# Performance work log

Hardware: AMD Instinct MI355X
Metric: run time of the kernel (lower is better)

## Reference

```python
import jax, jax.numpy as jnp
import numpy as np

DIM = 256; HEADS = 8; DK = 64; DV = 64; FH = 32; FW = 32; B = 16
INK = HEADS * DK; INV = HEADS * DV; N = FH * FW
SCALE = DK ** -0.5; EPS = 1e-5


def _pos_indices():
    pos = np.stack(np.meshgrid(np.arange(FH), np.arange(FW), indexing='ij'), axis=-1).reshape(-1, 2)
    rel = np.abs(pos[:, None, :] - pos[None, :, :])  # [N,N,2]
    return jnp.asarray(rel[..., 0] * FW + rel[..., 1], jnp.int32)  # [N,N]


def _bn(x, g, b, m, v):
    # eval-mode BatchNorm2d over channel axis 1
    s = (g / jnp.sqrt(v + EPS))
    return x * s[None, :, None, None] + (b - m * s)[None, :, None, None]


def setup_inputs() -> dict:
    key = jax.random.key(0)
    ks = jax.random.split(key, 24)
    f32 = jnp.float32
    def bn_params(k, c):
        k1, k2, k3, k4 = jax.random.split(k, 4)
        return (jax.random.normal(k1, (c,), f32) * 0.1 + 1.0,
                jax.random.normal(k2, (c,), f32) * 0.1,
                jax.random.normal(k3, (c,), f32) * 0.1,
                jax.random.uniform(k4, (c,), f32) + 0.5)
    gq, bq, mq, vq = bn_params(ks[1], INK)
    gk, bk, mk, vk = bn_params(ks[3], INK)
    gv, bv, mv, vv = bn_params(ks[5], INV)
    go, bo, mo, vo = bn_params(ks[7], DIM)
    return {
        'x': jax.random.normal(ks[0], (B, DIM, FH, FW), f32),
        'wq': jax.random.normal(ks[2], (INK, DIM), f32) * (DIM ** -0.5),
        'gq': gq, 'bq': bq, 'mq': mq, 'vq': vq,
        'wk': jax.random.normal(ks[4], (INK, DIM), f32) * (DIM ** -0.5),
        'gk': gk, 'bk': bk, 'mk': mk, 'vk': vk,
        'wv': jax.random.normal(ks[6], (INV, DIM), f32) * (DIM ** -0.5),
        'gv': gv, 'bv': bv, 'mv': mv, 'vv': vv,
        'emb': jax.random.normal(ks[8], (N, HEADS), f32) * 0.02,
        'w_out': jax.random.normal(ks[9], (DIM, INV), f32) * (INV ** -0.5),
        'b_out': jax.random.normal(ks[10], (DIM,), f32) * 0.02,
        'go': go, 'bo': bo, 'mo': mo, 'vo': vo,
        'pos_indices': _pos_indices(),
    }


def reference(x, wq, gq, bq, mq, vq, wk, gk, bk, mk, vk, wv, gv, bv, mv, vv,
              emb, w_out, b_out, go, bo, mo, vo, pos_indices):
    b = x.shape[0]
    # 1x1 conv == channel matmul
    q = _bn(jnp.einsum('bchw,oc->bohw', x, wq), gq, bq, mq, vq)
    k = _bn(jnp.einsum('bchw,oc->bohw', x, wk), gk, bk, mk, vk)
    v = _bn(jnp.einsum('bchw,oc->bohw', x, wv), gv, bv, mv, vv)
    # 'b (h d) x y -> b h (x y) d'
    def split_heads(t, d):
        return t.reshape(b, HEADS, d, N).transpose(0, 1, 3, 2)
    q = split_heads(q, DK); k = split_heads(k, DK); v = split_heads(v, DV)
    dots = jnp.einsum('bhid,bhjd->bhij', q, k) * SCALE  # [b,h,N,N]
    bias = emb[pos_indices]                               # [N,N,h] gather
    dots = dots + jnp.transpose(bias, (2, 0, 1))[None] / SCALE
    attn = jax.nn.softmax(dots, axis=-1)
    out = jnp.einsum('bhij,bhjd->bhid', attn, v)
    out = out.transpose(0, 1, 3, 2).reshape(b, INV, FH, FW)  # 'b h (x y) d -> b (h d) x y'
    hs = out * jnp.clip(out + 3.0, 0.0, 6.0) / 6.0           # Hardswish
    y = jnp.einsum('bchw,oc->bohw', hs, w_out) + b_out[None, :, None, None]
    return _bn(y, go, bo, mo, vo)
```

## Files before the change

### kernel.cpp

```cpp
#include <hip/hip_runtime.h>

typedef __attribute__((ext_vector_type(4))) float f32x4;
typedef __attribute__((ext_vector_type(8))) _Float16 f16x8;
typedef __attribute__((ext_vector_type(4))) _Float16 f16x4;

static __device__ __forceinline__ f32x4 mfma16f(f16x8 a, f16x8 b, f32x4 c) {
    return __builtin_amdgcn_mfma_f32_16x16x32_f16(a, b, c, 0, 0, 0);
}

__global__ __launch_bounds__(256) void prep(
    const float* __restrict__ x,
    const float* __restrict__ s0, const float* __restrict__ s1,
    const float* __restrict__ s2, const float* __restrict__ s3,
    _Float16* __restrict__ d0h, _Float16* __restrict__ d0l,
    _Float16* __restrict__ d1h, _Float16* __restrict__ d1l,
    _Float16* __restrict__ d2h, _Float16* __restrict__ d2l,
    _Float16* __restrict__ d3h, _Float16* __restrict__ d3l,
    _Float16* __restrict__ xth, _Float16* __restrict__ xtl)
{
    __shared__ float lt[32][36];
    const int t = threadIdx.x;
    const int bid = blockIdx.x;
    if (bid < 2048) {
        const int seg = bid >> 9;
        const int i = (bid & 511) * 256 + t;
        const float* src = (seg == 0) ? s0 : (seg == 1) ? s1 : (seg == 2) ? s2 : s3;
        _Float16* dh = (seg == 0) ? d0h : (seg == 1) ? d1h : (seg == 2) ? d2h : d3h;
        _Float16* dl = (seg == 0) ? d0l : (seg == 1) ? d1l : (seg == 2) ? d2l : d3l;
        const float f = src[i];
        const _Float16 h = (_Float16)f;
        dh[i] = h;
        dl[i] = (_Float16)(f - (float)h);
    } else {
        const int bid2 = bid - 2048;
        const int c0 = (bid2 & 7) * 32, hw0 = ((bid2 >> 3) & 31) * 32, b = bid2 >> 8;
        {
            const int cl = t >> 3, hw4 = (t & 7) * 4;
            *(f32x4*)&lt[cl][hw4] = *(const f32x4*)&x[((size_t)(b * 256 + c0 + cl)) * 1024 + hw0 + hw4];
        }
        __syncthreads();
        {
            const int hwl = t >> 3, c4 = (t & 7) * 4;
            f16x4 hv, lv;
#pragma unroll
            for (int e = 0; e < 4; ++e) {
                const float f = lt[c4 + e][hwl];
                const _Float16 h = (_Float16)f;
                hv[e] = h;
                lv[e] = (_Float16)(f - (float)h);
            }
            const size_t off = ((size_t)(b * 1024 + hw0 + hwl)) * 256 + c0 + c4;
            *(f16x4*)(xth + off) = hv;
            *(f16x4*)(xtl + off) = lv;
        }
    }
}

__global__ __launch_bounds__(256) void qkv_mfma(
    const _Float16* __restrict__ xth, const _Float16* __restrict__ xtl,
    const _Float16* __restrict__ wqh, const _Float16* __restrict__ wql,
    const _Float16* __restrict__ wkh, const _Float16* __restrict__ wkl,
    const _Float16* __restrict__ wvh, const _Float16* __restrict__ wvl,
    const float* __restrict__ gq, const float* __restrict__ bq, const float* __restrict__ mq, const float* __restrict__ vq,
    const float* __restrict__ gk, const float* __restrict__ bk, const float* __restrict__ mk, const float* __restrict__ vk,
    const float* __restrict__ gv, const float* __restrict__ bv, const float* __restrict__ mv, const float* __restrict__ vv,
    _Float16* __restrict__ qh, _Float16* __restrict__ ql,
    _Float16* __restrict__ kh,
    _Float16* __restrict__ vt)
{
    __shared__ _Float16 Ah[128][72];
    __shared__ _Float16 Al[128][72];
    __shared__ float sc_l[128], tc_l[128];

    const int t = threadIdx.x;
    const int bn = blockIdx.x;
    const int m0 = blockIdx.y * 128;
    const int proj = bn >> 2;
    const int o0 = (bn & 3) * 128;
    const int bimg = m0 >> 10;
    const int nb = m0 & 1023;

    const _Float16* Wh = (proj == 0) ? wqh : (proj == 1) ? wkh : wvh;
    const _Float16* Wl = (proj == 0) ? wql : (proj == 1) ? wkl : wvl;
    const float* G  = (proj == 0) ? gq : (proj == 1) ? gk : gv;
    const float* Bt = (proj == 0) ? bq : (proj == 1) ? bk : bv;
    const float* Mn = (proj == 0) ? mq : (proj == 1) ? mk : mv;
    const float* Vr = (proj == 0) ? vq : (proj == 1) ? vk : vv;

    if (t < 128) {
        const int o = o0 + t;
        float s = G[o] / sqrtf(Vr[o] + 1e-5f);
        float tt = Bt[o] - Mn[o] * s;
        if (proj == 0) { s *= 0.125f; tt *= 0.125f; }
        sc_l[t] = s; tc_l[t] = tt;
    }

    const int wave = t >> 6, lane = t & 63;
    const int quad = lane >> 4, l16 = lane & 15;
    const int wm = (wave >> 1) * 64, wn = (wave & 1) * 64;

    f32x4 acc[4][4] = {};

    for (int c0 = 0; c0 < 256; c0 += 64) {
        __syncthreads();
        {
            int r = t >> 3;
            const int cs = (t & 7) * 8;
#pragma unroll
            for (int p = 0; p < 4; ++p, r += 32) {
                const size_t off = ((size_t)(bimg * 1024 + nb + r)) * 256 + c0 + cs;
                *(f16x8*)&Ah[r][cs] = *(const f16x8*)(xth + off);
                *(f16x8*)&Al[r][cs] = *(const f16x8*)(xtl + off);
            }
        }
        __syncthreads();
#pragma unroll
        for (int kk = 0; kk < 2; ++kk) {
            f16x8 ah[4], al[4], bh[4], bl[4];
#pragma unroll
            for (int mi = 0; mi < 4; ++mi) {
                ah[mi] = *(const f16x8*)&Ah[wm + mi * 16 + l16][kk * 32 + quad * 8];
                al[mi] = *(const f16x8*)&Al[wm + mi * 16 + l16][kk * 32 + quad * 8];
            }
#pragma unroll
            for (int nj = 0; nj < 4; ++nj) {
                const size_t off = ((size_t)(o0 + wn + nj * 16 + l16)) * 256 + c0 + kk * 32 + quad * 8;
                bh[nj] = *(const f16x8*)(Wh + off);
                if (proj < 2) bl[nj] = *(const f16x8*)(Wl + off);
            }
            if (proj < 2) {
#pragma unroll
                for (int nj = 0; nj < 4; ++nj)
#pragma unroll
                    for (int mi = 0; mi < 4; ++mi) {
                        acc[nj][mi] = mfma16f(bh[nj], ah[mi], acc[nj][mi]);
                        acc[nj][mi] = mfma16f(bh[nj], al[mi], acc[nj][mi]);
                        acc[nj][mi] = mfma16f(bl[nj], ah[mi], acc[nj][mi]);
                    }
            } else {
#pragma unroll
                for (int mi = 0; mi < 4; ++mi)
#pragma unroll
                    for (int nj = 0; nj < 4; ++nj) {
                        acc[mi][nj] = mfma16f(ah[mi], bh[nj], acc[mi][nj]);
                        acc[mi][nj] = mfma16f(al[mi], bh[nj], acc[mi][nj]);
                    }
            }
        }
    }

    if (proj < 2) {
        _Float16* Oh = (proj == 0) ? qh : kh;
#pragma unroll
        for (int nj = 0; nj < 4; ++nj) {
            const int olb = wn + nj * 16 + quad * 4;
            const int ob = o0 + olb;
            const int head = ob >> 6, d0 = ob & 63;
#pragma unroll
            for (int mi = 0; mi < 4; ++mi) {
                const int n = nb + wm + mi * 16 + l16;
                f16x4 hv, lv;
#pragma unroll
                for (int rr = 0; rr < 4; ++rr) {
                    const float val = acc[nj][mi][rr] * sc_l[olb + rr] + tc_l[olb + rr];
                    const _Float16 h = (_Float16)val;
                    hv[rr] = h;
                    lv[rr] = (_Float16)(val - (float)h);
                }
                const size_t off = (((size_t)(bimg * 8 + head)) * 1024 + n) * 64 + d0;
                *(f16x4*)(Oh + off) = hv;
                if (proj == 0) *(f16x4*)(ql + off) = lv;
            }
        }
    } else {
#pragma unroll
        for (int nj = 0; nj < 4; ++nj) {
            const int olb = wn + nj * 16 + l16;
            const int o = o0 + olb;
            const int head = o >> 6, d = o & 63;
            const float s = sc_l[olb], tt = tc_l[olb];
#pragma unroll
            for (int mi = 0; mi < 4; ++mi) {
                const int n0 = nb + wm + mi * 16 + quad * 4;
                f16x4 v4;
#pragma unroll
                for (int rr = 0; rr < 4; ++rr) v4[rr] = (_Float16)(acc[mi][nj][rr] * s + tt);
                *(f16x4*)(vt + (((size_t)(bimg * 8 + head)) * 64 + d) * 1024 + n0) = v4;
            }
        }
    }
}

__global__ __launch_bounds__(256, 3) void attn_mfma(
    const _Float16* __restrict__ qh, const _Float16* __restrict__ ql,
    const _Float16* __restrict__ kh,
    const _Float16* __restrict__ vt,
    const float* __restrict__ emb,
    _Float16* __restrict__ hsh)
{
    __shared__ float    emb_s[1024];
    __shared__ _Float16 kth[64][76];
    __shared__ _Float16 vts[64][76];
    __shared__ _Float16 pt[128][76];

    const int t = threadIdx.x;
    const int bid = blockIdx.x;
    const int bh = bid & 127, qb = bid >> 7;
    const int b = bh >> 3, h = bh & 7;
    const int wave = t >> 6, lane = t & 63;
    const int quad = lane >> 4, l16 = lane & 15;
    const int q0 = qb * 128 + wave * 32;
    const float L2E = 1.44269504f;

    for (int i = t; i < 1024; i += 256) emb_s[i] = (8.0f * emb[i * 8 + h] - 12.0f) * L2E;

    const size_t base = (size_t)bh * 65536;

    f16x8 qfh[2][2], qfl[2][2];
#pragma unroll
    for (int mi = 0; mi < 2; ++mi)
#pragma unroll
        for (int kk = 0; kk < 2; ++kk) {
            const size_t off = base + (size_t)(q0 + mi * 16 + l16) * 64 + kk * 32 + quad * 8;
            qfh[mi][kk] = *(const f16x8*)(qh + off);
            qfl[mi][kk] = *(const f16x8*)(ql + off);
        }

    int xiv[2][4], dy0[2][4], dy1[2][4];
#pragma unroll
    for (int mi = 0; mi < 2; ++mi)
#pragma unroll
        for (int r = 0; r < 4; ++r) {
            const int ig = q0 + mi * 16 + quad * 4 + r;
            const int xi = ig >> 5, yi = ig & 31;
            xiv[mi][r] = xi;
            dy0[mi][r] = abs(yi - l16);
            dy1[mi][r] = abs(yi - 16 - l16);
        }

    const int sr = t >> 3;
    const int scs = (t & 7) * 8;
    const int rv = t >> 2;
    const int cv = (t & 3) * 16;

    f16x8 pkh[2], pvv[2];
#pragma unroll
    for (int p = 0; p < 2; ++p) {
        pkh[p] = *(const f16x8*)(kh + base + (size_t)(p * 32 + sr) * 64 + scs);
        pvv[p] = *(const f16x8*)(vt + base + (size_t)rv * 1024 + cv + p * 8);
    }

    f32x4 ao[2][4] = {};
    float lsum[2][4] = {};

    for (int jb = 0; jb < 16; ++jb) {
        __syncthreads();
#pragma unroll
        for (int p = 0; p < 2; ++p) {
            *(f16x8*)&kth[p * 32 + sr][scs] = pkh[p];
            *(f16x8*)&vts[rv][cv + p * 8] = pvv[p];
        }
        __syncthreads();
        if (jb < 15) {
#pragma unroll
            for (int p = 0; p < 2; ++p) {
                pkh[p] = *(const f16x8*)(kh + base + (size_t)((jb + 1) * 64 + p * 32 + sr) * 64 + scs);
                pvv[p] = *(const f16x8*)(vt + base + (size_t)rv * 1024 + (jb + 1) * 64 + cv + p * 8);
            }
        }

        f32x4 as[2][4] = {};
#pragma unroll
        for (int kk = 0; kk < 2; ++kk) {
            f16x8 kfh[4];
#pragma unroll
            for (int nj = 0; nj < 4; ++nj)
                kfh[nj] = *(const f16x8*)&kth[nj * 16 + l16][kk * 32 + quad * 8];
#pragma unroll
            for (int mi = 0; mi < 2; ++mi)
#pragma unroll
                for (int nj = 0; nj < 4; ++nj) {
                    as[mi][nj] = mfma16f(qfh[mi][kk], kfh[nj], as[mi][nj]);
                    as[mi][nj] = mfma16f(qfl[mi][kk], kfh[nj], as[mi][nj]);
                }
        }

        const int xj0 = jb * 2, xj1 = jb * 2 + 1;
#pragma unroll
        for (int mi = 0; mi < 2; ++mi) {
#pragma unroll
            for (int r = 0; r < 4; ++r) {
                const int dxa = abs(xiv[mi][r] - xj0) << 5;
                const int dxb = abs(xiv[mi][r] - xj1) << 5;
                const int prow = wave * 32 + mi * 16 + quad * 4 + r;
                const float p0 = exp2f(fmaf(as[mi][0][r], L2E, emb_s[dxa + dy0[mi][r]]));
                const float p1 = exp2f(fmaf(as[mi][1][r], L2E, emb_s[dxa + dy1[mi][r]]));
                const float p2 = exp2f(fmaf(as[mi][2][r], L2E, emb_s[dxb + dy0[mi][r]]));
                const float p3 = exp2f(fmaf(as[mi][3][r], L2E, emb_s[dxb + dy1[mi][r]]));
                lsum[mi][r] += (p0 + p1) + (p2 + p3);
                pt[prow][0 * 16 + l16] = (_Float16)p0;
                pt[prow][1 * 16 + l16] = (_Float16)p1;
                pt[prow][2 * 16 + l16] = (_Float16)p2;
                pt[prow][3 * 16 + l16] = (_Float16)p3;
            }
        }

#pragma unroll
        for (int kk = 0; kk < 2; ++kk) {
            f16x8 pa[2], vf[4];
#pragma unroll
            for (int mi = 0; mi < 2; ++mi)
                pa[mi] = *(const f16x8*)&pt[wave * 32 + mi * 16 + l16][kk * 32 + quad * 8];
#pragma unroll
            for (int dj = 0; dj < 4; ++dj)
                vf[dj] = *(const f16x8*)&vts[dj * 16 + l16][kk * 32 + quad * 8];
#pragma unroll
            for (int mi = 0; mi < 2; ++mi)
#pragma unroll
                for (int dj = 0; dj < 4; ++dj)
                    ao[mi][dj] = mfma16f(pa[mi], vf[dj], ao[mi][dj]);
        }
    }

#pragma unroll
    for (int mi = 0; mi < 2; ++mi) {
#pragma unroll
        for (int r = 0; r < 4; ++r) {
            float l = lsum[mi][r];
#pragma unroll
            for (int msk = 1; msk < 16; msk <<= 1)
                l += __shfl_xor(l, msk, 64);
            const float inv = 1.0f / l;
            const int ig = q0 + mi * 16 + quad * 4 + r;
#pragma unroll
            for (int dj = 0; dj < 4; ++dj) {
                const float o = ao[mi][dj][r] * inv;
                const float hsw = o * fminf(fmaxf(o + 3.0f, 0.0f), 6.0f) * (1.0f / 6.0f);
                hsh[((size_t)(b * 1024 + ig)) * 512 + h * 64 + dj * 16 + l16] = (_Float16)hsw;
            }
        }
    }
}

__global__ __launch_bounds__(256) void out_mfma(
    const _Float16* __restrict__ hsh,
    const _Float16* __restrict__ woh, const _Float16* __restrict__ wol,
    const float* __restrict__ b_out, const float* __restrict__ go, const float* __restrict__ bo,
    const float* __restrict__ mo, const float* __restrict__ vo, float* __restrict__ y)
{
    __shared__ _Float16 Ah[64][136];

    const int t = threadIdx.x;
    const int m0 = blockIdx.x * 64;
    const int o0 = blockIdx.y * 128;
    const int bimg = m0 >> 10, nb = m0 & 1023;
    const int wave = t >> 6, lane = t & 63;
    const int quad = lane >> 4, l16 = lane & 15;
    const int wm = (wave >> 1) * 32, wn = (wave & 1) * 64;

    f32x4 acc[2][4] = {};
    f16x8 bh[4], bl[4], nbh[4], nbl[4];

#pragma unroll
    for (int nj = 0; nj < 4; ++nj) {
        const size_t off = ((size_t)(o0 + wn + nj * 16 + l16)) * 512 + quad * 8;
        bh[nj] = *(const f16x8*)(woh + off);
        bl[nj] = *(const f16x8*)(wol + off);
    }

#pragma unroll
    for (int it = 0; it < 16; ++it) {
        const int c0 = (it >> 2) * 128, kk = it & 3;
        if (kk == 0) {
            __syncthreads();
            const int cs = (t & 7) * 16;
#pragma unroll
            for (int p = 0; p < 2; ++p) {
                const int r = (t >> 3) + p * 32;
                *(f16x8*)&Ah[r][cs]     = *(const f16x8*)(hsh + ((size_t)(m0 + r)) * 512 + c0 + cs);
                *(f16x8*)&Ah[r][cs + 8] = *(const f16x8*)(hsh + ((size_t)(m0 + r)) * 512 + c0 + cs + 8);
            }
            __syncthreads();
        }
        if (it < 15) {
            const int nit = it + 1;
            const int nc0 = (nit >> 2) * 128, nkk = nit & 3;
#pragma unroll
            for (int nj = 0; nj < 4; ++nj) {
                const size_t off = ((size_t)(o0 + wn + nj * 16 + l16)) * 512 + nc0 + nkk * 32 + quad * 8;
                nbh[nj] = *(const f16x8*)(woh + off);
                nbl[nj] = *(const f16x8*)(wol + off);
            }
        }
        f16x8 ah[2];
#pragma unroll
        for (int mi = 0; mi < 2; ++mi)
            ah[mi] = *(const f16x8*)&Ah[wm + mi * 16 + l16][kk * 32 + quad * 8];
#pragma unroll
        for (int mi = 0; mi < 2; ++mi)
#pragma unroll
            for (int nj = 0; nj < 4; ++nj) {
                acc[mi][nj] = mfma16f(ah[mi], bh[nj], acc[mi][nj]);
                acc[mi][nj] = mfma16f(ah[mi], bl[nj], acc[mi][nj]);
            }
#pragma unroll
        for (int nj = 0; nj < 4; ++nj) { bh[nj] = nbh[nj]; bl[nj] = nbl[nj]; }
    }

#pragma unroll
    for (int nj = 0; nj < 4; ++nj) {
        const int o = o0 + wn + nj * 16 + l16;
        const float s = go[o] / sqrtf(vo[o] + 1e-5f);
        const float tt = bo[o] - mo[o] * s;
        const float bf = b_out[o];
#pragma unroll
        for (int mi = 0; mi < 2; ++mi) {
            const int hw = nb + wm + mi * 16 + quad * 4;
            f32x4 v4;
#pragma unroll
            for (int rr = 0; rr < 4; ++rr) v4[rr] = (acc[mi][nj][rr] + bf) * s + tt;
            *(f32x4*)&y[((size_t)(bimg * 256 + o)) * 1024 + hw] = v4;
        }
    }
}

extern "C" void kernel_launch(void* const* d_in, const int* in_sizes, int n_in,
                              void* d_out, int out_size, void* d_ws, size_t ws_size,
                              hipStream_t stream) {
    const float* x     = (const float*)d_in[0];
    const float* wq    = (const float*)d_in[1];
    const float* gq    = (const float*)d_in[2];
    const float* bq    = (const float*)d_in[3];
    const float* mq    = (const float*)d_in[4];
    const float* vq    = (const float*)d_in[5];
    const float* wk    = (const float*)d_in[6];
    const float* gk    = (const float*)d_in[7];
    const float* bk    = (const float*)d_in[8];
    const float* mk    = (const float*)d_in[9];
    const float* vk    = (const float*)d_in[10];
    const float* wv    = (const float*)d_in[11];
    const float* gv    = (const float*)d_in[12];
    const float* bv    = (const float*)d_in[13];
    const float* mv    = (const float*)d_in[14];
    const float* vv    = (const float*)d_in[15];
    const float* emb   = (const float*)d_in[16];
    const float* w_out = (const float*)d_in[17];
    const float* b_out = (const float*)d_in[18];
    const float* go    = (const float*)d_in[19];
    const float* bo    = (const float*)d_in[20];
    const float* mo    = (const float*)d_in[21];
    const float* vo    = (const float*)d_in[22];

    _Float16* us = (_Float16*)d_ws;
    _Float16* xth = us;
    _Float16* xtl = us + 4194304;
    _Float16* hsh = us;
    _Float16* wsp = us + 16777216;
    _Float16* wqh = wsp,            *wql = wsp + 131072;
    _Float16* wkh = wsp + 262144,   *wkl = wsp + 393216;
    _Float16* wvh = wsp + 524288,   *wvl = wsp + 655360;
    _Float16* woh = wsp + 786432,   *wol = wsp + 917504;
    _Float16* qv  = us + 17825792;
    _Float16* qhw = qv,             *qlw = qv + 8388608;
    _Float16* khw = qv + 16777216;
    _Float16* vtw = qv + 33554432;

    prep<<<6144, 256, 0, stream>>>(x, wq, wk, wv, w_out,
                                   wqh, wql, wkh, wkl, wvh, wvl, woh, wol,
                                   xth, xtl);

    qkv_mfma<<<dim3(12, 128), 256, 0, stream>>>(
        xth, xtl, wqh, wql, wkh, wkl, wvh, wvl,
        gq, bq, mq, vq, gk, bk, mk, vk, gv, bv, mv, vv,
        qhw, qlw, khw, vtw);

    attn_mfma<<<1024, 256, 0, stream>>>(
        qhw, qlw, khw, vtw, emb, hsh);

    out_mfma<<<dim3(256, 2), 256, 0, stream>>>(
        hsh, woh, wol, b_out, go, bo, mo, vo, (float*)d_out);
}
```

Before: 304.6 us.

## Compute transposed scores so softmax probs feed PV MFMA from registers

The QK^T MFMA now takes K as the A operand and Q as the B operand. The resulting transposed score fragment lines up directly with the A-operand layout of a 16x16x16 f16 MFMA for the P·V product. This removes the shared-memory P tile (pt) and its store/load round-trip, and cuts LDS use, which may raise occupancy. In exchange it uses the smaller-K 16x16x16 MFMA, gathers emb_s with per-element index math, and reworks the row-sum reduction with extra shuffles.

```diff
diff --git a/kernel.cpp b/kernel.cpp
--- a/kernel.cpp
+++ b/kernel.cpp
@@ -201,7 +201,6 @@
     __shared__ float    emb_s[1024];
     __shared__ _Float16 kth[64][76];
     __shared__ _Float16 vts[64][76];
-    __shared__ _Float16 pt[128][76];
 
     const int t = threadIdx.x;
     const int bid = blockIdx.x;
@@ -226,17 +225,13 @@
             qfl[mi][kk] = *(const f16x8*)(ql + off);
         }
 
-    int xiv[2][4], dy0[2][4], dy1[2][4];
-#pragma unroll
-    for (int mi = 0; mi < 2; ++mi)
-#pragma unroll
-        for (int r = 0; r < 4; ++r) {
-            const int ig = q0 + mi * 16 + quad * 4 + r;
-            const int xi = ig >> 5, yi = ig & 31;
-            xiv[mi][r] = xi;
-            dy0[mi][r] = abs(yi - l16);
-            dy1[mi][r] = abs(yi - 16 - l16);
-        }
+    int xi[2], yi[2];
+#pragma unroll
+    for (int mi = 0; mi < 2; ++mi) {
+        const int ig = q0 + mi * 16 + l16;
+        xi[mi] = ig >> 5;
+        yi[mi] = ig & 31;
+    }
 
     const int sr = t >> 3;
     const int scs = (t & 7) * 8;
@@ -251,7 +246,7 @@
     }
 
     f32x4 ao[2][4] = {};
-    float lsum[2][4] = {};
+    float lsum[2] = {};
 
     for (int jb = 0; jb < 16; ++jb) {
         __syncthreads();
@@ -269,72 +264,65 @@
             }
         }
 
-        f32x4 as[2][4] = {};
-#pragma unroll
-        for (int kk = 0; kk < 2; ++kk) {
-            f16x8 kfh[4];
-#pragma unroll
-            for (int nj = 0; nj < 4; ++nj)
-                kfh[nj] = *(const f16x8*)&kth[nj * 16 + l16][kk * 32 + quad * 8];
+#pragma unroll
+        for (int nj = 0; nj < 4; ++nj) {
+            const f16x8 kf0 = *(const f16x8*)&kth[nj * 16 + l16][quad * 8];
+            const f16x8 kf1 = *(const f16x8*)&kth[nj * 16 + l16][32 + quad * 8];
+
+            f32x4 ss[2] = {};
+#pragma unroll
+            for (int mi = 0; mi < 2; ++mi) {
+                ss[mi] = mfma16f(kf0, qfh[mi][0], ss[mi]);
+                ss[mi] = mfma16f(kf0, qfl[mi][0], ss[mi]);
+                ss[mi] = mfma16f(kf1, qfh[mi][1], ss[mi]);
+                ss[mi] = mfma16f(kf1, qfl[mi][1], ss[mi]);
+            }
+
+            const int xj = 2 * jb + (nj >> 1);
+            const int yj0 = ((nj & 1) << 4) + quad * 4;
+            f16x4 pa[2];
+#pragma unroll
+            for (int mi = 0; mi < 2; ++mi) {
+                const int dxo = abs(xi[mi] - xj) << 5;
+                const int yq = yi[mi] - yj0;
+                const float p0 = exp2f(fmaf(ss[mi][0], L2E, emb_s[dxo + abs(yq)]));
+                const float p1 = exp2f(fmaf(ss[mi][1], L2E, emb_s[dxo + abs(yq - 1)]));
+                const float p2 = exp2f(fmaf(ss[mi][2], L2E, emb_s[dxo + abs(yq - 2)]));
+                const float p3 = exp2f(fmaf(ss[mi][3], L2E, emb_s[dxo + abs(yq - 3)]));
+                lsum[mi] += (p0 + p1) + (p2 + p3);
+                f16x4 pv;
+                pv[0] = (_Float16)p0; pv[1] = (_Float16)p1;
+                pv[2] = (_Float16)p2; pv[3] = (_Float16)p3;
+                pa[mi] = pv;
+            }
+
+            f16x4 vf[4];
+#pragma unroll
+            for (int dj = 0; dj < 4; ++dj)
+                vf[dj] = *(const f16x4*)&vts[dj * 16 + l16][nj * 16 + quad * 4];
 #pragma unroll
             for (int mi = 0; mi < 2; ++mi)
 #pragma unroll
-                for (int nj = 0; nj < 4; ++nj) {
-                    as[mi][nj] = mfma16f(qfh[mi][kk], kfh[nj], as[mi][nj]);
-                    as[mi][nj] = mfma16f(qfl[mi][kk], kfh[nj], as[mi][nj]);
-                }
-        }
-
-        const int xj0 = jb * 2, xj1 = jb * 2 + 1;
-#pragma unroll
-        for (int mi = 0; mi < 2; ++mi) {
-#pragma unroll
-            for (int r = 0; r < 4; ++r) {
-                const int dxa = abs(xiv[mi][r] - xj0) << 5;
-                const int dxb = abs(xiv[mi][r] - xj1) << 5;
-                const int prow = wave * 32 + mi * 16 + quad * 4 + r;
-                const float p0 = exp2f(fmaf(as[mi][0][r], L2E, emb_s[dxa + dy0[mi][r]]));
-                const float p1 = exp2f(fmaf(as[mi][1][r], L2E, emb_s[dxa + dy1[mi][r]]));
-                const float p2 = exp2f(fmaf(as[mi][2][r], L2E, emb_s[dxb + dy0[mi][r]]));
-                const float p3 = exp2f(fmaf(as[mi][3][r], L2E, emb_s[dxb + dy1[mi][r]]));
-                lsum[mi][r] += (p0 + p1) + (p2 + p3);
-                pt[prow][0 * 16 + l16] = (_Float16)p0;
-                pt[prow][1 * 16 + l16] = (_Float16)p1;
-                pt[prow][2 * 16 + l16] = (_Float16)p2;
-                pt[prow][3 * 16 + l16] = (_Float16)p3;
-            }
-        }
-
-#pragma unroll
-        for (int kk = 0; kk < 2; ++kk) {
-            f16x8 pa[2], vf[4];
-#pragma unroll
-            for (int mi = 0; mi < 2; ++mi)
-                pa[mi] = *(const f16x8*)&pt[wave * 32 + mi * 16 + l16][kk * 32 + quad * 8];
-#pragma unroll
-            for (int dj = 0; dj < 4; ++dj)
-                vf[dj] = *(const f16x8*)&vts[dj * 16 + l16][kk * 32 + quad * 8];
-#pragma unroll
-            for (int mi = 0; mi < 2; ++mi)
-#pragma unroll
                 for (int dj = 0; dj < 4; ++dj)
-                    ao[mi][dj] = mfma16f(pa[mi], vf[dj], ao[mi][dj]);
+                    ao[mi][dj] = __builtin_amdgcn_mfma_f32_16x16x16f16(pa[mi], vf[dj], ao[mi][dj], 0, 0, 0);
         }
     }
 
 #pragma unroll
     for (int mi = 0; mi < 2; ++mi) {
+        float l = lsum[mi];
+        l += __shfl_xor(l, 16, 64);
+        l += __shfl_xor(l, 32, 64);
+        float inv[4];
+#pragma unroll
+        for (int r = 0; r < 4; ++r)
+            inv[r] = 1.0f / __shfl(l, quad * 4 + r, 64);
 #pragma unroll
         for (int r = 0; r < 4; ++r) {
-            float l = lsum[mi][r];
-#pragma unroll
-            for (int msk = 1; msk < 16; msk <<= 1)
-                l += __shfl_xor(l, msk, 64);
-            const float inv = 1.0f / l;
             const int ig = q0 + mi * 16 + quad * 4 + r;
 #pragma unroll
             for (int dj = 0; dj < 4; ++dj) {
-                const float o = ao[mi][dj][r] * inv;
+                const float o = ao[mi][dj][r] * inv[r];
                 const float hsw = o * fminf(fmaxf(o + 3.0f, 0.0f), 6.0f) * (1.0f / 6.0f);
                 hsh[((size_t)(b * 1024 + ig)) * 512 + h * 64 + dj * 16 + l16] = (_Float16)hsw;
             }
```

Measured after the change: 299.5 us. Within noise of the previous version (-1.7%).
